# Optimization experiments

Hardware: AMD Instinct MI355X
Metric: run time of the kernel (lower is better)

## Reference

```python
import jax, jax.numpy as jnp
import numpy as np

N_NODES = 100000
N_EDGES = 1600000
N_GRAPHS = 512
F_IN = 128
HID = 128
N_CLS = 10


def setup_inputs() -> dict:
    key = jax.random.key(0)
    ks = jax.random.split(key, 8)
    s = 1.0 / np.sqrt(HID)
    x = jax.random.normal(ks[0], (N_NODES, F_IN), dtype=jnp.float32)
    edge_index = jax.random.randint(ks[1], (2, N_EDGES), 0, N_NODES, dtype=jnp.int64)
    batch = jnp.sort(jax.random.randint(ks[2], (N_NODES,), 0, N_GRAPHS, dtype=jnp.int64))
    W0 = jax.random.normal(ks[3], (F_IN, HID), dtype=jnp.float32) * s
    W1 = jax.random.normal(ks[4], (HID, HID), dtype=jnp.float32) * s
    W2 = jax.random.normal(ks[5], (HID, HID), dtype=jnp.float32) * s
    Wl = jax.random.normal(ks[6], (HID, N_CLS), dtype=jnp.float32) * s
    return {
        'x': x, 'edge_index': edge_index, 'batch': batch,
        'W0': W0, 'b0': jnp.zeros((HID,), jnp.float32),
        'W1': W1, 'b1': jnp.zeros((HID,), jnp.float32),
        'W2': W2, 'b2': jnp.zeros((HID,), jnp.float32),
        'Wl': Wl, 'bl': jnp.zeros((N_CLS,), jnp.float32),
    }


def reference(x, edge_index, batch, W0, b0, W1, b1, W2, b2, Wl, bl):
    N = x.shape[0]
    # GCN: add self-loops, symmetric normalization D^-1/2 (A+I) D^-1/2
    loops = jnp.arange(N, dtype=edge_index.dtype)
    row = jnp.concatenate([edge_index[0], loops])  # source
    col = jnp.concatenate([edge_index[1], loops])  # target
    deg = jax.ops.segment_sum(jnp.ones_like(col, dtype=x.dtype), col, num_segments=N)
    dinv = jax.lax.rsqrt(jnp.maximum(deg, 1.0))  # deg >= 1 after self-loops
    norm = dinv[row] * dinv[col]  # [E+N]

    def gcn(h, W, b):
        h = h @ W                       # [N, H] linear transform first (fewer edge flops)
        msg = h[row] * norm[:, None]    # gather + normalize
        return jax.ops.segment_sum(msg, col, num_segments=N) + b  # scatter-add

    h = jax.nn.relu(gcn(x, W0, b0))
    h = jax.nn.relu(gcn(h, W1, b1))
    h = jax.nn.relu(gcn(h, W2, b2))

    # global_mean_pool over graphs
    counts = jax.ops.segment_sum(jnp.ones((N,), x.dtype), batch, num_segments=N_GRAPHS)
    pooled = jax.ops.segment_sum(h, batch, num_segments=N_GRAPHS) / jnp.maximum(counts, 1.0)[:, None]
    return pooled @ Wl + bl
```

## Files before the change

### kernel.cpp

```cpp
#include <hip/hip_runtime.h>
#include <hip/hip_bf16.h>

#define ELL_D 64

typedef __attribute__((ext_vector_type(8))) short short8;
typedef __attribute__((ext_vector_type(8))) unsigned short ushort8;
typedef __attribute__((ext_vector_type(4))) float f32x4;

__device__ __forceinline__ unsigned short f2bf(float f) {
    __hip_bfloat16 h = __float2bfloat16(f);
    return *(unsigned short*)&h;
}
__device__ __forceinline__ float bf2f(unsigned short u) {
    unsigned int v = ((unsigned int)u) << 16;
    return __uint_as_float(v);
}


__device__ __forceinline__ void gemm_body(int bid, const float* __restrict__ H,
                                          const float* __restrict__ W, unsigned short* __restrict__ A,
                                          int N, float4* wl4) {
    int tid = threadIdx.x;
    const float4* __restrict__ W4 = (const float4*)W;
    int tc = tid & 15;
    int tr = tid >> 4;
    int rbase = bid * 64 + tr * 4;

    const float4* __restrict__ H4 = (const float4*)H;
    float acc[4][8] = {};
    int r[4];
#pragma unroll
    for (int j = 0; j < 4; j++) {
        int rr = rbase + j;
        r[j] = (rr < N) ? rr : (N - 1);
    }

    for (int p = 0; p < 2; p++) {
        if (p) __syncthreads();
#pragma unroll
        for (int i = 0; i < 8; i++) wl4[i * 256 + tid] = W4[p * 2048 + i * 256 + tid];
        __syncthreads();
#pragma unroll 4
        for (int k4 = 0; k4 < 16; k4++) {
            union { float4 v; float f[4]; } hu[4];
#pragma unroll
            for (int j = 0; j < 4; j++) hu[j].v = H4[r[j] * 32 + p * 16 + k4];
#pragma unroll
            for (int kk = 0; kk < 4; kk++) {
                float4 w0 = wl4[(k4 * 4 + kk) * 32 + tc];
                float4 w1 = wl4[(k4 * 4 + kk) * 32 + 16 + tc];
#pragma unroll
                for (int j = 0; j < 4; j++) {
                    float h = hu[j].f[kk];
                    acc[j][0] = fmaf(h, w0.x, acc[j][0]);
                    acc[j][1] = fmaf(h, w0.y, acc[j][1]);
                    acc[j][2] = fmaf(h, w0.z, acc[j][2]);
                    acc[j][3] = fmaf(h, w0.w, acc[j][3]);
                    acc[j][4] = fmaf(h, w1.x, acc[j][4]);
                    acc[j][5] = fmaf(h, w1.y, acc[j][5]);
                    acc[j][6] = fmaf(h, w1.z, acc[j][6]);
                    acc[j][7] = fmaf(h, w1.w, acc[j][7]);
                }
            }
        }
    }

    ushort4* __restrict__ A4 = (ushort4*)A;
#pragma unroll
    for (int j = 0; j < 4; j++) {
        int rr = rbase + j;
        if (rr < N) {
            A4[rr * 32 + tc]      = make_ushort4(f2bf(acc[j][0]), f2bf(acc[j][1]), f2bf(acc[j][2]), f2bf(acc[j][3]));
            A4[rr * 32 + 16 + tc] = make_ushort4(f2bf(acc[j][4]), f2bf(acc[j][5]), f2bf(acc[j][6]), f2bf(acc[j][7]));
        }
    }
}


__device__ __forceinline__ void fill_body(int bid, const int* __restrict__ col, const int* __restrict__ row,
                                          int* __restrict__ cnt, int* __restrict__ ell, int E) {
    int t = bid * 256 + threadIdx.x;
    int base = t * 8;
    if (base + 8 <= E) {
        int4 ca = *(const int4*)(col + base);
        int4 cb = *(const int4*)(col + base + 4);
        int4 ra = *(const int4*)(row + base);
        int4 rb = *(const int4*)(row + base + 4);
        int p0 = atomicAdd(&cnt[ca.x], 1) & 63;
        int p1 = atomicAdd(&cnt[ca.y], 1) & 63;
        int p2 = atomicAdd(&cnt[ca.z], 1) & 63;
        int p3 = atomicAdd(&cnt[ca.w], 1) & 63;
        int p4 = atomicAdd(&cnt[cb.x], 1) & 63;
        int p5 = atomicAdd(&cnt[cb.y], 1) & 63;
        int p6 = atomicAdd(&cnt[cb.z], 1) & 63;
        int p7 = atomicAdd(&cnt[cb.w], 1) & 63;
        ell[ca.x * ELL_D + p0] = ra.x;
        ell[ca.y * ELL_D + p1] = ra.y;
        ell[ca.z * ELL_D + p2] = ra.z;
        ell[ca.w * ELL_D + p3] = ra.w;
        ell[cb.x * ELL_D + p4] = rb.x;
        ell[cb.y * ELL_D + p5] = rb.y;
        ell[cb.z * ELL_D + p6] = rb.z;
        ell[cb.w * ELL_D + p7] = rb.w;
    } else {
        for (int e = base; e < E; e++) {
            int c = col[e];
            int pos = atomicAdd(&cnt[c], 1) & 63;
            ell[c * ELL_D + pos] = row[e];
        }
    }
}

__device__ __forceinline__ void prep_wt_body(int which, const float* __restrict__ W1, const float* __restrict__ W2,
                                             unsigned short* __restrict__ WT1, unsigned short* __restrict__ WT2) {
    const float* W = which ? W2 : W1;
    unsigned short* WT = which ? WT2 : WT1;
    for (int i = threadIdx.x; i < 16384; i += 256) {
        int c = i >> 7, k = i & 127;
        WT[i] = f2bf(W[k * 128 + c]);
    }
}

__global__ __launch_bounds__(256) void k_fused(const float* __restrict__ H, const float* __restrict__ W,
                                               unsigned short* __restrict__ A,
                                               const int* __restrict__ col, const int* __restrict__ row,
                                               int* __restrict__ cnt, int* __restrict__ ell,
                                               const float* __restrict__ W1, const float* __restrict__ W2,
                                               unsigned short* __restrict__ WT1, unsigned short* __restrict__ WT2,
                                               int N, int E, int gb, int fb) {
    __shared__ float4 wl4[2048];
    int b = blockIdx.x;
    if (b < 2) { prep_wt_body(b, W1, W2, WT1, WT2); return; }
    b -= 2;
    int half = b >> 1;
    if (!(b & 1)) {
        if (half < gb) gemm_body(half, H, W, A, N, wl4);
    } else {
        if (half < fb) fill_body(half, col, row, cnt, ell, E);
    }
}


__global__ __launch_bounds__(256) void k_scaleA_pad(const int* __restrict__ cnt, float* __restrict__ dinv,
                                                    unsigned short* __restrict__ A, int* __restrict__ ell, int N) {
    int node = blockIdx.x * 8 + (threadIdx.x >> 5);
    int li = threadIdx.x & 31;
    if (node < N) {
        int deg = cnt[node];
        float dn = 1.0f / sqrtf((float)(deg + 1));
        if (deg > 63) deg = 63;
        if (li == 0) dinv[node] = dn;
        ushort4* Ap = (ushort4*)A + (size_t)node * 32 + li;
        ushort4 v = *Ap;
        v.x = f2bf(bf2f(v.x) * dn);
        v.y = f2bf(bf2f(v.y) * dn);
        v.z = f2bf(bf2f(v.z) * dn);
        v.w = f2bf(bf2f(v.w) * dn);
        *Ap = v;
        int pend = (deg + 8) & ~7;
        if (pend > 64) pend = 64;
        int* er = ell + (size_t)node * ELL_D;
        if (li == 0) er[deg] = node;
        else if (li < 8 && deg + li < pend) er[deg + li] = N;
    }
    if (blockIdx.x == 0 && threadIdx.x < 32) {
        ((ushort4*)A)[(size_t)N * 32 + threadIdx.x] = make_ushort4(0, 0, 0, 0);
    }
}


__global__ __launch_bounds__(256) void k_agg(const unsigned short* __restrict__ Ain, const int* __restrict__ cnt,
                                             const int* __restrict__ ell, const float* __restrict__ dinv,
                                             const float* __restrict__ bias, unsigned short* __restrict__ Bout, int N) {
    int tid = threadIdx.x;
    int li = tid & 15;
    int n = blockIdx.x * 16 + (tid >> 4);
    if (n >= N) return;
    const ushort8* __restrict__ A8 = (const ushort8*)Ain;
    int deg = cnt[n];
    if (deg > 63) deg = 63;
    int pend = (deg + 8) & ~7;
    if (pend > 64) pend = 64;
    int nq = pend >> 2;
    const int4* __restrict__ l4 = (const int4*)(ell + (size_t)n * ELL_D);

    float a0 = 0.f, a1 = 0.f, a2 = 0.f, a3 = 0.f, a4 = 0.f, a5 = 0.f, a6 = 0.f, a7 = 0.f;
    for (int q = 0; q < nq; q += 2) {
        int4 qa = l4[q], qb = l4[q + 1];
        ushort8 v0 = A8[(size_t)qa.x * 16 + li];
        ushort8 v1 = A8[(size_t)qa.y * 16 + li];
        ushort8 v2 = A8[(size_t)qa.z * 16 + li];
        ushort8 v3 = A8[(size_t)qa.w * 16 + li];
        ushort8 v4 = A8[(size_t)qb.x * 16 + li];
        ushort8 v5 = A8[(size_t)qb.y * 16 + li];
        ushort8 v6 = A8[(size_t)qb.z * 16 + li];
        ushort8 v7 = A8[(size_t)qb.w * 16 + li];
        a0 += (bf2f(v0[0]) + bf2f(v1[0])) + (bf2f(v2[0]) + bf2f(v3[0])) + (bf2f(v4[0]) + bf2f(v5[0])) + (bf2f(v6[0]) + bf2f(v7[0]));
        a1 += (bf2f(v0[1]) + bf2f(v1[1])) + (bf2f(v2[1]) + bf2f(v3[1])) + (bf2f(v4[1]) + bf2f(v5[1])) + (bf2f(v6[1]) + bf2f(v7[1]));
        a2 += (bf2f(v0[2]) + bf2f(v1[2])) + (bf2f(v2[2]) + bf2f(v3[2])) + (bf2f(v4[2]) + bf2f(v5[2])) + (bf2f(v6[2]) + bf2f(v7[2]));
        a3 += (bf2f(v0[3]) + bf2f(v1[3])) + (bf2f(v2[3]) + bf2f(v3[3])) + (bf2f(v4[3]) + bf2f(v5[3])) + (bf2f(v6[3]) + bf2f(v7[3]));
        a4 += (bf2f(v0[4]) + bf2f(v1[4])) + (bf2f(v2[4]) + bf2f(v3[4])) + (bf2f(v4[4]) + bf2f(v5[4])) + (bf2f(v6[4]) + bf2f(v7[4]));
        a5 += (bf2f(v0[5]) + bf2f(v1[5])) + (bf2f(v2[5]) + bf2f(v3[5])) + (bf2f(v4[5]) + bf2f(v5[5])) + (bf2f(v6[5]) + bf2f(v7[5]));
        a6 += (bf2f(v0[6]) + bf2f(v1[6])) + (bf2f(v2[6]) + bf2f(v3[6])) + (bf2f(v4[6]) + bf2f(v5[6])) + (bf2f(v6[6]) + bf2f(v7[6]));
        a7 += (bf2f(v0[7]) + bf2f(v1[7])) + (bf2f(v2[7]) + bf2f(v3[7])) + (bf2f(v4[7]) + bf2f(v5[7])) + (bf2f(v6[7]) + bf2f(v7[7]));
    }
    float dn = dinv[n];
    const float4* __restrict__ b4 = (const float4*)bias;
    float4 bl0 = b4[li * 2], bl1 = b4[li * 2 + 1];
    ushort8 o;
    o[0] = f2bf(fmaxf(fmaf(a0, dn, bl0.x), 0.f));
    o[1] = f2bf(fmaxf(fmaf(a1, dn, bl0.y), 0.f));
    o[2] = f2bf(fmaxf(fmaf(a2, dn, bl0.z), 0.f));
    o[3] = f2bf(fmaxf(fmaf(a3, dn, bl0.w), 0.f));
    o[4] = f2bf(fmaxf(fmaf(a4, dn, bl1.x), 0.f));
    o[5] = f2bf(fmaxf(fmaf(a5, dn, bl1.y), 0.f));
    o[6] = f2bf(fmaxf(fmaf(a6, dn, bl1.z), 0.f));
    o[7] = f2bf(fmaxf(fmaf(a7, dn, bl1.w), 0.f));
    ((ushort8*)Bout)[(size_t)n * 16 + li] = o;
}


__global__ __launch_bounds__(256) void k_gemm_mfma(const unsigned short* __restrict__ H,
                                                   const unsigned short* __restrict__ WT,
                                                   const float* __restrict__ dinv,
                                                   unsigned short* __restrict__ A, int N) {
    __shared__ float ep[4 * 16 * 132];
    int tid = threadIdx.x, w = tid >> 6, l = tid & 63;
    int rbase = blockIdx.x * 64 + w * 16;
    int lrow = l & 15, lk = l >> 4;

    int r = rbase + lrow;
    if (r >= N) r = N - 1;
    const short8* __restrict__ Hp = (const short8*)(H + (size_t)r * 128);
    short8 af[4];
#pragma unroll
    for (int kc = 0; kc < 4; kc++) af[kc] = Hp[kc * 4 + lk];

    f32x4 acc[8];
#pragma unroll
    for (int t = 0; t < 8; t++) {
        f32x4 a = {0.f, 0.f, 0.f, 0.f};
        const short8* __restrict__ Wp = (const short8*)(WT + (size_t)(t * 16 + lrow) * 128);
#pragma unroll
        for (int kc = 0; kc < 4; kc++) {
            short8 bf = Wp[kc * 4 + lk];
            a = __builtin_amdgcn_mfma_f32_16x16x32_bf16(af[kc], bf, a, 0, 0, 0);
        }
        acc[t] = a;
    }

    float* base = ep + w * 2112;
#pragma unroll
    for (int t = 0; t < 8; t++)
#pragma unroll
        for (int j = 0; j < 4; j++)
            base[(4 * lk + j) * 132 + t * 16 + lrow] = acc[t][j];
    __syncthreads();

    int row16 = l >> 2, c0 = (l & 3) * 32;
    int orow = rbase + row16;
    if (orow < N) {
        float dn = dinv[orow];
        const float* src = base + row16 * 132 + c0;
        unsigned short* dst = A + (size_t)orow * 128 + c0;
#pragma unroll
        for (int q = 0; q < 4; q++) {
            union { short8 s8; unsigned short u[8]; } pk;
#pragma unroll
            for (int e = 0; e < 8; e++) pk.u[e] = f2bf(src[q * 8 + e] * dn);
            *(short8*)(dst + q * 8) = pk.s8;
        }
    }
}


__global__ __launch_bounds__(512) void k_pool(const unsigned short* __restrict__ B, const int* __restrict__ batch,
                                              const float* __restrict__ Wl, const float* __restrict__ bl,
                                              float* __restrict__ out, int N) {
    int g = blockIdx.x;
    int tid = threadIdx.x;
    int k8 = tid & 15, h = tid >> 4;
    __shared__ int se[2];
    __shared__ float red[32][128];
    if (tid < 2) {
        int target = g + tid;
        int lo = 0, hi = N;
        while (lo < hi) {
            int mid = (lo + hi) >> 1;
            if (batch[mid] < target) lo = mid + 1; else hi = mid;
        }
        se[tid] = lo;
    }
    __syncthreads();
    int start = se[0], end = se[1];
    float s[8] = {};
    for (int n = start + h; n < end; n += 32) {
        ushort8 v = *(const ushort8*)(B + (size_t)n * 128 + k8 * 8);
#pragma unroll
        for (int j = 0; j < 8; j++) s[j] += bf2f(v[j]);
    }
#pragma unroll
    for (int j = 0; j < 8; j++) red[h][k8 * 8 + j] = s[j];
    __syncthreads();
    for (int off = 16; off >= 1; off >>= 1) {
        if (h < off) {
#pragma unroll
            for (int j = 0; j < 8; j++) red[h][k8 * 8 + j] += red[h + off][k8 * 8 + j];
        }
        __syncthreads();
    }
    if (h == 0) {
        int cg = end - start;
        float inv = 1.0f / (float)(cg > 1 ? cg : 1);
#pragma unroll
        for (int j = 0; j < 8; j++) red[0][k8 * 8 + j] *= inv;
    }
    __syncthreads();
    if (tid < 10) {
        float o = bl[tid];
        for (int j = 0; j < 128; j++) o = fmaf(red[0][j], Wl[j * 10 + tid], o);
        out[g * 10 + tid] = o;
    }
}


extern "C" void kernel_launch(void* const* d_in, const int* in_sizes, int n_in,
                              void* d_out, int out_size, void* d_ws, size_t ws_size,
                              hipStream_t stream) {
    const float* x  = (const float*)d_in[0];
    const int* eidx = (const int*)d_in[1];
    const int* batch = (const int*)d_in[2];
    const float* W0 = (const float*)d_in[3];
    const float* b0 = (const float*)d_in[4];
    const float* W1 = (const float*)d_in[5];
    const float* b1 = (const float*)d_in[6];
    const float* W2 = (const float*)d_in[7];
    const float* b2 = (const float*)d_in[8];
    const float* Wl = (const float*)d_in[9];
    const float* bl = (const float*)d_in[10];

    int N = in_sizes[0] / 128;
    int E = in_sizes[1] / 2;
    int G = out_size / 10;
    const int* row = eidx;
    const int* col = eidx + E;

    char* w = (char*)d_ws;
    auto carve = [&](size_t bytes) -> void* {
        void* p = (void*)w;
        w += (bytes + 511) & ~(size_t)511;
        return p;
    };
    unsigned short* A  = (unsigned short*)carve((size_t)(N + 1) * 128 * 2);
    unsigned short* Bb = (unsigned short*)carve((size_t)N * 128 * 2);
    int*   cnt  = (int*)carve((size_t)N * 4);
    float* dinv = (float*)carve((size_t)N * 4);
    int*   ell  = (int*)carve((size_t)N * ELL_D * 4);
    unsigned short* WT1 = (unsigned short*)carve(16384 * 2);
    unsigned short* WT2 = (unsigned short*)carve(16384 * 2);

    int gb = (N + 63) / 64;
    int ft = (E + 7) / 8;
    int fb = (ft + 255) / 256;
    int M  = (gb > fb) ? gb : fb;

    hipMemsetAsync(cnt, 0, (size_t)N * 4, stream);
    k_fused<<<2 * M + 2, 256, 0, stream>>>(x, W0, A, col, row, cnt, ell, W1, W2, WT1, WT2, N, E, gb, fb);
    k_scaleA_pad<<<(N + 7) / 8, 256, 0, stream>>>(cnt, dinv, A, ell, N);

    int ab = (N + 15) / 16;
    int mb = (N + 63) / 64;
    k_agg<<<ab, 256, 0, stream>>>(A, cnt, ell, dinv, b0, Bb, N);
    k_gemm_mfma<<<mb, 256, 0, stream>>>(Bb, WT1, dinv, A, N);
    k_agg<<<ab, 256, 0, stream>>>(A, cnt, ell, dinv, b1, Bb, N);
    k_gemm_mfma<<<mb, 256, 0, stream>>>(Bb, WT2, dinv, A, N);
    k_agg<<<ab, 256, 0, stream>>>(A, cnt, ell, dinv, b2, Bb, N);
    k_pool<<<G, 512, 0, stream>>>(Bb, batch, Wl, bl, (float*)d_out, N);
}
```

Measured before the change: 381.4 us.

## Pipeline aggregation and GEMM across node chunks in a combined kernel

Merges the aggregation and MFMA GEMM kernels into one launch that splits blocks between aggregating node chunk j and running the GEMM on chunk j-1. This lets the two stages overlap and fill the tail of each launch, with a second A buffer so the GEMM output does not overwrite aggregation input. The GEMM epilogue now applies dinv and converts to bf16 before staging in shared memory, which halves LDS use and drops the float round trip. The cost is more kernel launches (K+1 per layer) and extra workspace.

Result: slower. 405.0 us (+6.2%).

```diff
diff --git a/kernel.cpp b/kernel.cpp
--- a/kernel.cpp
+++ b/kernel.cpp
@@ -169,13 +169,14 @@
 }
 
 
-__global__ __launch_bounds__(256) void k_agg(const unsigned short* __restrict__ Ain, const int* __restrict__ cnt,
-                                             const int* __restrict__ ell, const float* __restrict__ dinv,
-                                             const float* __restrict__ bias, unsigned short* __restrict__ Bout, int N) {
+__device__ __forceinline__ void agg_body(int bid, const unsigned short* __restrict__ Ain,
+                                         const int* __restrict__ cnt, const int* __restrict__ ell,
+                                         const float* __restrict__ dinv, const float* __restrict__ bias,
+                                         unsigned short* __restrict__ Bout, int alo, int ahi, int N) {
     int tid = threadIdx.x;
     int li = tid & 15;
-    int n = blockIdx.x * 16 + (tid >> 4);
-    if (n >= N) return;
+    int n = alo + bid * 16 + (tid >> 4);
+    if (n >= ahi) return;
     const ushort8* __restrict__ A8 = (const ushort8*)Ain;
     int deg = cnt[n];
     if (deg > 63) deg = 63;
@@ -220,56 +221,70 @@
 }
 
 
-__global__ __launch_bounds__(256) void k_gemm_mfma(const unsigned short* __restrict__ H,
-                                                   const unsigned short* __restrict__ WT,
-                                                   const float* __restrict__ dinv,
-                                                   unsigned short* __restrict__ A, int N) {
-    __shared__ float ep[4 * 16 * 132];
+__device__ __forceinline__ void gemm_mfma_body(int bid, const unsigned short* __restrict__ H,
+                                               const unsigned short* __restrict__ WT,
+                                               const float* __restrict__ dinv,
+                                               unsigned short* __restrict__ Ag,
+                                               int glo, int ghi, int N, unsigned short* ep) {
     int tid = threadIdx.x, w = tid >> 6, l = tid & 63;
-    int rbase = blockIdx.x * 64 + w * 16;
-    int lrow = l & 15, lk = l >> 4;
-
-    int r = rbase + lrow;
+    int rbase = glo + bid * 64 + w * 16;
+    int lcol = l & 15, lk = l >> 4;
+
+    int r = rbase + lcol;
     if (r >= N) r = N - 1;
     const short8* __restrict__ Hp = (const short8*)(H + (size_t)r * 128);
     short8 af[4];
 #pragma unroll
     for (int kc = 0; kc < 4; kc++) af[kc] = Hp[kc * 4 + lk];
 
-    f32x4 acc[8];
+    float dnr[4];
+#pragma unroll
+    for (int j = 0; j < 4; j++) {
+        int rr = rbase + w * 0 + 4 * lk + j;
+        dnr[j] = dinv[(rr < N) ? rr : (N - 1)];
+    }
+
+    unsigned short* base = ep + w * 2176;
 #pragma unroll
     for (int t = 0; t < 8; t++) {
         f32x4 a = {0.f, 0.f, 0.f, 0.f};
-        const short8* __restrict__ Wp = (const short8*)(WT + (size_t)(t * 16 + lrow) * 128);
+        const short8* __restrict__ Wp = (const short8*)(WT + (size_t)(t * 16 + lcol) * 128);
 #pragma unroll
         for (int kc = 0; kc < 4; kc++) {
             short8 bf = Wp[kc * 4 + lk];
             a = __builtin_amdgcn_mfma_f32_16x16x32_bf16(af[kc], bf, a, 0, 0, 0);
         }
-        acc[t] = a;
-    }
-
-    float* base = ep + w * 2112;
-#pragma unroll
-    for (int t = 0; t < 8; t++)
 #pragma unroll
         for (int j = 0; j < 4; j++)
-            base[(4 * lk + j) * 132 + t * 16 + lrow] = acc[t][j];
+            base[(4 * lk + j) * 136 + t * 16 + lcol] = f2bf(a[j] * dnr[j]);
+    }
     __syncthreads();
 
     int row16 = l >> 2, c0 = (l & 3) * 32;
     int orow = rbase + row16;
-    if (orow < N) {
-        float dn = dinv[orow];
-        const float* src = base + row16 * 132 + c0;
-        unsigned short* dst = A + (size_t)orow * 128 + c0;
-#pragma unroll
-        for (int q = 0; q < 4; q++) {
-            union { short8 s8; unsigned short u[8]; } pk;
-#pragma unroll
-            for (int e = 0; e < 8; e++) pk.u[e] = f2bf(src[q * 8 + e] * dn);
-            *(short8*)(dst + q * 8) = pk.s8;
-        }
+    if (orow < ghi) {
+        const unsigned short* src = base + row16 * 136 + c0;
+        unsigned short* dst = Ag + (size_t)orow * 128 + c0;
+#pragma unroll
+        for (int q = 0; q < 4; q++)
+            *(short8*)(dst + q * 8) = *(const short8*)(src + q * 8);
+    }
+}
+
+
+__global__ __launch_bounds__(256) void k_pipe(const unsigned short* __restrict__ Ain,
+                                              const int* __restrict__ cnt, const int* __restrict__ ell,
+                                              const float* __restrict__ dinv, const float* __restrict__ bias,
+                                              unsigned short* __restrict__ Bout, int alo, int ahi, int nab,
+                                              const unsigned short* __restrict__ Hg,
+                                              const unsigned short* __restrict__ WT,
+                                              unsigned short* __restrict__ Ag, int glo, int ghi, int N) {
+    __shared__ unsigned short ep[4 * 16 * 136];
+    int b = blockIdx.x;
+    if (b < nab) {
+        agg_body(b, Ain, cnt, ell, dinv, bias, Bout, alo, ahi, N);
+    } else {
+        gemm_mfma_body(b - nab, Hg, WT, dinv, Ag, glo, ghi, N, ep);
     }
 }
 
@@ -346,18 +361,22 @@
     const int* col = eidx + E;
 
     char* w = (char*)d_ws;
+    size_t used = 0;
     auto carve = [&](size_t bytes) -> void* {
-        void* p = (void*)w;
-        w += (bytes + 511) & ~(size_t)511;
+        void* p = (void*)(w + used);
+        used += (bytes + 511) & ~(size_t)511;
         return p;
     };
-    unsigned short* A  = (unsigned short*)carve((size_t)(N + 1) * 128 * 2);
+    unsigned short* A1 = (unsigned short*)carve((size_t)(N + 1) * 128 * 2);
     unsigned short* Bb = (unsigned short*)carve((size_t)N * 128 * 2);
     int*   cnt  = (int*)carve((size_t)N * 4);
     float* dinv = (float*)carve((size_t)N * 4);
     int*   ell  = (int*)carve((size_t)N * ELL_D * 4);
     unsigned short* WT1 = (unsigned short*)carve(16384 * 2);
     unsigned short* WT2 = (unsigned short*)carve(16384 * 2);
+    size_t a2_bytes = ((size_t)(N + 1) * 128 * 2 + 511) & ~(size_t)511;
+    bool canPipe = (used + a2_bytes) <= ws_size;
+    unsigned short* A2 = canPipe ? (unsigned short*)carve((size_t)(N + 1) * 128 * 2) : A1;
 
     int gb = (N + 63) / 64;
     int ft = (E + 7) / 8;
@@ -365,15 +384,36 @@
     int M  = (gb > fb) ? gb : fb;
 
     hipMemsetAsync(cnt, 0, (size_t)N * 4, stream);
-    k_fused<<<2 * M + 2, 256, 0, stream>>>(x, W0, A, col, row, cnt, ell, W1, W2, WT1, WT2, N, E, gb, fb);
-    k_scaleA_pad<<<(N + 7) / 8, 256, 0, stream>>>(cnt, dinv, A, ell, N);
-
+    k_fused<<<2 * M + 2, 256, 0, stream>>>(x, W0, A1, col, row, cnt, ell, W1, W2, WT1, WT2, N, E, gb, fb);
+    k_scaleA_pad<<<(N + 7) / 8, 256, 0, stream>>>(cnt, dinv, A1, ell, N);
+
+    auto run_pair = [&](const unsigned short* Ain, const float* bias, const unsigned short* WT,
+                        unsigned short* Ag, int K) {
+        int C = (((N + K - 1) / K) + 63) & ~(int)63;
+        for (int j = 0; j <= K; j++) {
+            int alo = j * C, ahi = alo + C;
+            if (alo > N) alo = N;
+            if (ahi > N) ahi = N;
+            int glo = (j - 1) * C, ghi = glo + C;
+            if (j == 0) { glo = 0; ghi = 0; }
+            if (ghi > N) ghi = N;
+            int nab = (ahi > alo) ? (ahi - alo + 15) / 16 : 0;
+            int ngb = (ghi > glo) ? (ghi - glo + 63) / 64 : 0;
+            if (nab + ngb == 0) continue;
+            k_pipe<<<nab + ngb, 256, 0, stream>>>(Ain, cnt, ell, dinv, bias, Bb, alo, ahi, nab,
+                                                  Bb, WT, Ag, glo, ghi, N);
+        }
+    };
+
+    if (canPipe) {
+        run_pair(A1, b0, WT1, A2, 4);
+        run_pair(A2, b1, WT2, A1, 4);
+    } else {
+        run_pair(A1, b0, WT1, A1, 1);
+        run_pair(A1, b1, WT2, A1, 1);
+    }
     int ab = (N + 15) / 16;
-    int mb = (N + 63) / 64;
-    k_agg<<<ab, 256, 0, stream>>>(A, cnt, ell, dinv, b0, Bb, N);
-    k_gemm_mfma<<<mb, 256, 0, stream>>>(Bb, WT1, dinv, A, N);
-    k_agg<<<ab, 256, 0, stream>>>(A, cnt, ell, dinv, b1, Bb, N);
-    k_gemm_mfma<<<mb, 256, 0, stream>>>(Bb, WT2, dinv, A, N);
-    k_agg<<<ab, 256, 0, stream>>>(A, cnt, ell, dinv, b2, Bb, N);
+    unsigned short* A3 = canPipe ? A1 : A1;
+    k_pipe<<<ab, 256, 0, stream>>>(A3, cnt, ell, dinv, b2, Bb, 0, N, ab, Bb, WT1, A2, 0, 0, N);
     k_pool<<<G, 512, 0, stream>>>(Bb, batch, Wl, bl, (float*)d_out, N);
 }
```
